# Kernel tuning notes

Measured on AMD Instinct MI355X. Metric: run time of the kernel, lower is better.

The kernel has to match this reference:

```python
import jax, jax.numpy as jnp
import numpy as np

N = 50000        # nodes
E = 800000       # edges (avg degree 16)
F_IN = 128       # in_features
F_OUT = 64       # out_features per head
HEADS = 4        # SparseGATConv default n_heads
ALPHA = 0.01     # LeakyReLU negative slope (SparseGATConv default alpha)


def setup_inputs() -> dict:
    key = jax.random.key(0)
    ks = jax.random.split(key, 6)
    x = jax.random.normal(ks[0], (N, F_IN), dtype=jnp.float32)
    edge_index = jax.random.randint(ks[1], (2, E), 0, N, dtype=jnp.int64)
    # xavier-normal-ish init, gain 1.414 as in the torch module
    W_heads = jax.random.normal(ks[2], (HEADS, F_IN, F_OUT), dtype=jnp.float32) * (1.414 / np.sqrt(F_IN))
    attn_heads = jax.random.normal(ks[3], (HEADS, 2 * F_OUT, 1), dtype=jnp.float32) * 0.1
    W_out = jax.random.normal(ks[4], (HEADS * F_OUT, F_OUT), dtype=jnp.float32) * (1.414 / np.sqrt(HEADS * F_OUT))
    attn_out = jax.random.normal(ks[5], (2 * F_OUT, 1), dtype=jnp.float32) * 0.1
    return {"x": x, "edge_index": edge_index, "W_heads": W_heads,
            "attn_heads": attn_heads, "W_out": W_out, "attn_out": attn_out}


def _sp_gat_layer(x, src, dst, W, attn, concat):
    """SpGraphAttentionLayer.forward: dense x @ W, edge attention scores,
    sparse row-softmax over COO adjacency, sparse-mm aggregation."""
    h = x @ W                                   # (N, d)
    d = h.shape[1]
    # cat(h[src], h[dst]) @ attn  ==  (h@a1)[src] + (h@a2)[dst]  (avoids (E,2d) concat)
    s1 = (h @ attn[:d]).squeeze(-1)             # (N,)
    s2 = (h @ attn[d:]).squeeze(-1)             # (N,)
    scores = -jax.nn.leaky_relu(s1[src] + s2[dst], negative_slope=ALPHA)  # (E,)
    # torch.sparse.softmax(dim=1): softmax over existing entries in each row (src)
    row_max = jax.ops.segment_max(scores, src, num_segments=N)
    ex = jnp.exp(scores - row_max[src])
    denom = jax.ops.segment_sum(ex, src, num_segments=N)
    a = ex / denom[src]                         # (E,) edge attention weights
    # sparse.mm: out[i] = sum_{e: src[e]=i} a[e] * h[dst[e]]
    out = jax.ops.segment_sum(a[:, None] * h[dst], src, num_segments=N)  # (N, d)
    return jax.nn.elu(out) if concat else out


def reference(x, edge_index, W_heads, attn_heads, W_out, attn_out):
    src, dst = edge_index[0], edge_index[1]
    # multi-head GAT layers (concat=True), then out_att on concatenated features
    heads_out = jax.vmap(lambda W, a: _sp_gat_layer(x, src, dst, W, a, True))(W_heads, attn_heads)  # (H, N, F_OUT)
    hcat = jnp.transpose(heads_out, (1, 0, 2)).reshape(N, HEADS * F_OUT)  # matches torch.cat(dim=1) head order
    return _sp_gat_layer(hcat, src, dst, W_out, attn_out, False)          # (N, F_OUT)
```

## Files before the change

### kernel.cpp

```cpp
#include <hip/hip_runtime.h>

typedef unsigned short u16;
typedef _Float16 f16;
typedef __attribute__((ext_vector_type(8))) _Float16 f16x8;
typedef __attribute__((ext_vector_type(2))) _Float16 f16x2;
typedef __attribute__((ext_vector_type(4))) float f32x4;

__device__ inline float nlrelu(float z) { return (z > 0.f) ? -z : -0.01f * z; }
__device__ inline float4 score4(float4 a, float4 b) {
    return make_float4(nlrelu(a.x + b.x), nlrelu(a.y + b.y), nlrelu(a.z + b.z), nlrelu(a.w + b.w));
}
__device__ inline unsigned packdup(float w) {
    f16x2 p = (f16x2){(f16)w, (f16)w};
    return __builtin_bit_cast(unsigned, p);
}

__global__ __launch_bounds__(256) void k_initcnt(const float* __restrict__ Wh, const float* __restrict__ Wo,
                       f16* __restrict__ B1, f16* __restrict__ B2,
                       const int* __restrict__ src, int* __restrict__ counts, int* __restrict__ pos,
                       int* __restrict__ cursor, int E, int N) {
    const int b = blockIdx.x;
    if (b == 0 && threadIdx.x == 0) *cursor = 0;
    if (b < 128) {
        int i = b * 256 + threadIdx.x;
        int j = i & 7, lane = (i >> 3) & 63, kg = (i >> 9) & 3, nt = i >> 11;
        int n = nt * 16 + (lane & 15);
        int k = kg * 32 + ((lane >> 4) << 3) + j;
        B1[i] = (f16)Wh[(n >> 6) * (128 * 64) + k * 64 + (n & 63)];
    } else if (b < 192) {
        int i = (b - 128) * 256 + threadIdx.x;
        int j = i & 7, lane = (i >> 3) & 63, kg = (i >> 9) & 7, nt = i >> 12;
        int n = nt * 16 + (lane & 15);
        int k = kg * 32 + ((lane >> 4) << 3) + j;
        B2[i] = (f16)Wo[k * 64 + n];
    } else {
        const int base = (b - 192) * 1024 + threadIdx.x;
#pragma unroll
        for (int j = 0; j < 4; j++) {
            int e = base + j * 256;
            if (e < E) {
                int s = src[e];
                s = ((unsigned)s < (unsigned)N) ? s : 0;
                pos[e] = atomicAdd(&counts[s], 1);
            }
        }
    }
}

__global__ __launch_bounds__(1024) void scan_ticket(const int* __restrict__ counts, int* __restrict__ rowst,
                                                    int* __restrict__ cursor, int n) {
    const int t = threadIdx.x, lane = t & 63, w = t >> 6;
    __shared__ int wsum[16];
    __shared__ int sh_base;
    int i = blockIdx.x * 1024 + t;
    int v = (i < n) ? counts[i] : 0;
    int orig = v;
    for (int d = 1; d < 64; d <<= 1) { int x = __shfl_up(v, d); if (lane >= d) v += x; }
    if (lane == 63) wsum[w] = v;
    __syncthreads();
    if (t == 0) {
        int acc = 0;
        for (int j = 0; j < 16; j++) { int tmp = wsum[j]; wsum[j] = acc; acc += tmp; }
        sh_base = atomicAdd(cursor, acc);
    }
    __syncthreads();
    if (i < n) rowst[i] = sh_base + wsum[w] + (v - orig);
}

__global__ __launch_bounds__(256) void scatter_noat(const int* __restrict__ src, const int* __restrict__ dst,
                                                    const int* __restrict__ rowst, const int* __restrict__ pos,
                                                    int* __restrict__ edged, int E, int N) {
    const int base = blockIdx.x * 1024 + threadIdx.x;
#pragma unroll
    for (int j = 0; j < 4; j++) {
        int e = base + j * 256;
        if (e < E) {
            int s = src[e];
            s = ((unsigned)s < (unsigned)N) ? s : 0;
            int d = dst[e];
            d = ((unsigned)d < (unsigned)N) ? d : 0;
            edged[rowst[s] + pos[e]] = d;
        }
    }
}

__global__ __launch_bounds__(256) void gemm1_f16(const float* __restrict__ X, const f16* __restrict__ B1,
        const float* __restrict__ attnH,
        f16* __restrict__ H1, float* __restrict__ s1, float* __restrict__ s2, int M) {
    const int lane = threadIdx.x & 63, wave = threadIdx.x >> 6;
    const int row0 = (blockIdx.x * 4 + wave) * 16;
    if (row0 >= M) return;
    const int mrow = row0 + (lane & 15);
    const int koff = (lane >> 4) * 8;
    const float* aptr = X + (size_t)mrow * 128 + koff;

    f32x4 acc[16];
#pragma unroll
    for (int c = 0; c < 16; c++) acc[c] = (f32x4){0.f, 0.f, 0.f, 0.f};

#pragma unroll
    for (int kg = 0; kg < 4; kg++) {
        float av[8];
        *(float4*)av       = *(const float4*)(aptr + kg * 32);
        *(float4*)(av + 4) = *(const float4*)(aptr + kg * 32 + 4);
        f16x8 a;
#pragma unroll
        for (int j = 0; j < 8; j++) a[j] = (f16)av[j];
#pragma unroll
        for (int nt = 0; nt < 16; nt++) {
            const size_t bidx = (size_t)(((nt << 2) + kg) * 64 + lane) * 8;
            f16x8 bfr = *(const f16x8*)(B1 + bidx);
            acc[nt] = __builtin_amdgcn_mfma_f32_16x16x32_f16(a, bfr, acc[nt], 0, 0, 0);
        }
    }
    const int rbase = (lane >> 4) * 4;
    const int colq = lane & 15;
#pragma unroll
    for (int h = 0; h < 4; h++) {
        float s1a[4] = {0.f, 0.f, 0.f, 0.f}, s2a[4] = {0.f, 0.f, 0.f, 0.f};
#pragma unroll
        for (int q = 0; q < 4; q++) {
            const int nt = h * 4 + q;
            const int col = nt * 16 + colq;
            const float a1v = attnH[h * 128 + (col & 63)];
            const float a2v = attnH[h * 128 + 64 + (col & 63)];
#pragma unroll
            for (int r = 0; r < 4; r++) {
                float c = acc[nt][r];
                H1[(size_t)(row0 + rbase + r) * 256 + col] = (f16)c;
                s1a[r] += c * a1v;
                s2a[r] += c * a2v;
            }
        }
#pragma unroll
        for (int off = 1; off < 16; off <<= 1)
#pragma unroll
            for (int r = 0; r < 4; r++) {
                s1a[r] += __shfl_xor(s1a[r], off);
                s2a[r] += __shfl_xor(s2a[r], off);
            }
        if (colq == 0)
#pragma unroll
            for (int r = 0; r < 4; r++) {
                s1[(size_t)(row0 + rbase + r) * 4 + h] = s1a[r];
                s2[(size_t)(row0 + rbase + r) * 4 + h] = s2a[r];
            }
    }
}

__global__ __launch_bounds__(256) void gemm2_f16(const f16* __restrict__ Hc, const f16* __restrict__ B2,
        const float* __restrict__ attnO,
        f16* __restrict__ H2, float* __restrict__ s1b, float* __restrict__ s2b, int M) {
    const int lane = threadIdx.x & 63, wave = threadIdx.x >> 6;
    const int row0 = (blockIdx.x * 4 + wave) * 16;
    if (row0 >= M) return;
    const int mrow = row0 + (lane & 15);
    const int koff = (lane >> 4) * 8;
    const f16* ap = Hc + (size_t)mrow * 256 + koff;

    f32x4 acc[4];
#pragma unroll
    for (int c = 0; c < 4; c++) acc[c] = (f32x4){0.f, 0.f, 0.f, 0.f};

#pragma unroll
    for (int kg = 0; kg < 8; kg++) {
        f16x8 a = *(const f16x8*)(ap + kg * 32);
#pragma unroll
        for (int nt = 0; nt < 4; nt++) {
            const size_t bidx = (size_t)(((nt << 3) + kg) * 64 + lane) * 8;
            f16x8 bfr = *(const f16x8*)(B2 + bidx);
            acc[nt] = __builtin_amdgcn_mfma_f32_16x16x32_f16(a, bfr, acc[nt], 0, 0, 0);
        }
    }
    const int rbase = (lane >> 4) * 4;
    const int colq = lane & 15;
    float s1a[4] = {0.f, 0.f, 0.f, 0.f}, s2a[4] = {0.f, 0.f, 0.f, 0.f};
#pragma unroll
    for (int nt = 0; nt < 4; nt++) {
        const int col = nt * 16 + colq;
        const float a1v = attnO[col];
        const float a2v = attnO[64 + col];
#pragma unroll
        for (int r = 0; r < 4; r++) {
            float c = acc[nt][r];
            H2[(size_t)(row0 + rbase + r) * 64 + col] = (f16)c;
            s1a[r] += c * a1v;
            s2a[r] += c * a2v;
        }
    }
#pragma unroll
    for (int off = 1; off < 16; off <<= 1)
#pragma unroll
        for (int r = 0; r < 4; r++) {
            s1a[r] += __shfl_xor(s1a[r], off);
            s2a[r] += __shfl_xor(s2a[r], off);
        }
    if (colq == 0)
#pragma unroll
        for (int r = 0; r < 4; r++) {
            s1b[row0 + rbase + r] = s1a[r];
            s2b[row0 + rbase + r] = s2a[r];
        }
}

__global__ __launch_bounds__(256) void agg_l1(const int* __restrict__ rowst, const int* __restrict__ cnt,
                                              const int* __restrict__ edged,
                                              const float* __restrict__ s1, const float* __restrict__ s2,
                                              const f16* __restrict__ H, f16* __restrict__ hcat, int N) {
    __shared__ unsigned wls[4][64][4];
    __shared__ int dls[4][64];
    const int t = threadIdx.x, lane = t & 63, wave = t >> 6;
    const int node = blockIdx.x * 4 + wave;
    if (node >= N) return;
    const int beg = rowst[node];
    const int deg = cnt[node];
    const int end = beg + deg;
    if (deg == 0) {
        *(uint2*)(hcat + (size_t)node * 256 + lane * 4) = make_uint2(0u, 0u);
        return;
    }
    const float4 s1v = *(const float4*)(s1 + (size_t)node * 4);

    if (deg <= 64) {
        int d = 0;
        if (lane < deg) d = edged[beg + lane];
        dls[wave][lane] = d;
        float4 s2v = *(const float4*)(s2 + (size_t)d * 4);
        float4 sc = score4(s1v, s2v);
        if (lane >= deg) sc = make_float4(-3e38f, -3e38f, -3e38f, -3e38f);
        float4 m = sc;
#pragma unroll
        for (int off = 32; off > 0; off >>= 1) {
            m.x = fmaxf(m.x, __shfl_xor(m.x, off));
            m.y = fmaxf(m.y, __shfl_xor(m.y, off));
            m.z = fmaxf(m.z, __shfl_xor(m.z, off));
            m.w = fmaxf(m.w, __shfl_xor(m.w, off));
        }
        float4 ex = make_float4(0.f, 0.f, 0.f, 0.f);
        if (lane < deg) ex = make_float4(__expf(sc.x - m.x), __expf(sc.y - m.y),
                                         __expf(sc.z - m.z), __expf(sc.w - m.w));
        float4 sm = ex;
#pragma unroll
        for (int off = 32; off > 0; off >>= 1) {
            sm.x += __shfl_xor(sm.x, off);
            sm.y += __shfl_xor(sm.y, off);
            sm.z += __shfl_xor(sm.z, off);
            sm.w += __shfl_xor(sm.w, off);
        }
        wls[wave][lane][0] = packdup(ex.x / sm.x);
        wls[wave][lane][1] = packdup(ex.y / sm.y);
        wls[wave][lane][2] = packdup(ex.z / sm.z);
        wls[wave][lane][3] = packdup(ex.w / sm.w);
        const int h2 = lane >> 5;
        const int p = lane & 31;
        const int headp = p >> 3;
        f16x2 a0[4], a1[4];
#pragma unroll
        for (int j = 0; j < 4; j++) { a0[j] = (f16x2)(f16)0.f; a1[j] = (f16x2)(f16)0.f; }
        for (int e = 0; e < deg; e += 2) {
            int ei = e + h2;
            int dd = dls[wave][ei];
            f16x2 w2 = __builtin_bit_cast(f16x2, wls[wave][ei][headp]);
            uint4 raw = *(const uint4*)(H + (size_t)dd * 256 + p * 8);
            if ((e >> 1) & 1) {
                a1[0] += w2 * __builtin_bit_cast(f16x2, raw.x);
                a1[1] += w2 * __builtin_bit_cast(f16x2, raw.y);
                a1[2] += w2 * __builtin_bit_cast(f16x2, raw.z);
                a1[3] += w2 * __builtin_bit_cast(f16x2, raw.w);
            } else {
                a0[0] += w2 * __builtin_bit_cast(f16x2, raw.x);
                a0[1] += w2 * __builtin_bit_cast(f16x2, raw.y);
                a0[2] += w2 * __builtin_bit_cast(f16x2, raw.z);
                a0[3] += w2 * __builtin_bit_cast(f16x2, raw.w);
            }
        }
        float r[8];
#pragma unroll
        for (int j = 0; j < 4; j++) {
            r[2 * j]     = (float)a0[j][0] + (float)a1[j][0];
            r[2 * j + 1] = (float)a0[j][1] + (float)a1[j][1];
        }
#pragma unroll
        for (int k = 0; k < 8; k++) r[k] += __shfl_xor(r[k], 32);
        if (lane < 32) {
            uint4 o;
            unsigned* op = &o.x;
#pragma unroll
            for (int j = 0; j < 4; j++) {
                float v0 = r[2 * j], v1 = r[2 * j + 1];
                v0 = (v0 > 0.f) ? v0 : (__expf(v0) - 1.f);
                v1 = (v1 > 0.f) ? v1 : (__expf(v1) - 1.f);
                f16x2 pk = (f16x2){(f16)v0, (f16)v1};
                op[j] = __builtin_bit_cast(unsigned, pk);
            }
            *(uint4*)(hcat + (size_t)node * 256 + p * 8) = o;
        }
    } else {
        const int head = lane >> 4;
        float4 m = make_float4(-3e38f, -3e38f, -3e38f, -3e38f);
        for (int e = beg + lane; e < end; e += 64) {
            int d = edged[e];
            float4 sc = score4(s1v, *(const float4*)(s2 + (size_t)d * 4));
            m.x = fmaxf(m.x, sc.x); m.y = fmaxf(m.y, sc.y); m.z = fmaxf(m.z, sc.z); m.w = fmaxf(m.w, sc.w);
        }
#pragma unroll
        for (int off = 32; off > 0; off >>= 1) {
            m.x = fmaxf(m.x, __shfl_xor(m.x, off));
            m.y = fmaxf(m.y, __shfl_xor(m.y, off));
            m.z = fmaxf(m.z, __shfl_xor(m.z, off));
            m.w = fmaxf(m.w, __shfl_xor(m.w, off));
        }
        float4 sm = make_float4(0.f, 0.f, 0.f, 0.f);
        for (int e = beg + lane; e < end; e += 64) {
            int d = edged[e];
            float4 sc = score4(s1v, *(const float4*)(s2 + (size_t)d * 4));
            sm.x += __expf(sc.x - m.x); sm.y += __expf(sc.y - m.y);
            sm.z += __expf(sc.z - m.z); sm.w += __expf(sc.w - m.w);
        }
#pragma unroll
        for (int off = 32; off > 0; off >>= 1) {
            sm.x += __shfl_xor(sm.x, off);
            sm.y += __shfl_xor(sm.y, off);
            sm.z += __shfl_xor(sm.z, off);
            sm.w += __shfl_xor(sm.w, off);
        }
        float4 inv = make_float4(1.f / sm.x, 1.f / sm.y, 1.f / sm.z, 1.f / sm.w);
        float4 acc = make_float4(0.f, 0.f, 0.f, 0.f);
        for (int e = beg; e < end; e++) {
            int dd = edged[e];
            float4 sc = score4(s1v, *(const float4*)(s2 + (size_t)dd * 4));
            float wv[4] = { __expf(sc.x - m.x) * inv.x, __expf(sc.y - m.y) * inv.y,
                            __expf(sc.z - m.z) * inv.z, __expf(sc.w - m.w) * inv.w };
            float w = (head == 0) ? wv[0] : (head == 1) ? wv[1] : (head == 2) ? wv[2] : wv[3];
            const f16* hp = H + (size_t)dd * 256 + lane * 4;
            acc.x += w * (float)hp[0]; acc.y += w * (float)hp[1];
            acc.z += w * (float)hp[2]; acc.w += w * (float)hp[3];
        }
        acc.x = (acc.x > 0.f) ? acc.x : (__expf(acc.x) - 1.f);
        acc.y = (acc.y > 0.f) ? acc.y : (__expf(acc.y) - 1.f);
        acc.z = (acc.z > 0.f) ? acc.z : (__expf(acc.z) - 1.f);
        acc.w = (acc.w > 0.f) ? acc.w : (__expf(acc.w) - 1.f);
        f16x2 o0 = (f16x2){(f16)acc.x, (f16)acc.y};
        f16x2 o1 = (f16x2){(f16)acc.z, (f16)acc.w};
        *(uint2*)(hcat + (size_t)node * 256 + lane * 4) =
            make_uint2(__builtin_bit_cast(unsigned, o0), __builtin_bit_cast(unsigned, o1));
    }
}

__global__ __launch_bounds__(256) void agg_l2(const int* __restrict__ rowst, const int* __restrict__ cnt,
                                              const int* __restrict__ edged,
                                              const float* __restrict__ s1, const float* __restrict__ s2,
                                              const f16* __restrict__ H, float* __restrict__ outp, int N) {
    __shared__ float wls[4][64];
    __shared__ int dls[4][64];
    const int t = threadIdx.x, lane = t & 63, wave = t >> 6;
    const int node = blockIdx.x * 4 + wave;
    if (node >= N) return;
    const int beg = rowst[node];
    const int deg = cnt[node];
    const int end = beg + deg;
    if (deg == 0) { outp[(size_t)node * 64 + lane] = 0.f; return; }
    const float s1v = s1[node];

    if (deg <= 64) {
        int d = 0;
        if (lane < deg) d = edged[beg + lane];
        dls[wave][lane] = d;
        float z = s1v + s2[d];
        float sc = (lane < deg) ? nlrelu(z) : -3e38f;
        float m = sc;
#pragma unroll
        for (int off = 32; off > 0; off >>= 1) m = fmaxf(m, __shfl_xor(m, off));
        float ex = (lane < deg) ? __expf(sc - m) : 0.f;
        float sm = ex;
#pragma unroll
        for (int off = 32; off > 0; off >>= 1) sm += __shfl_xor(sm, off);
        wls[wave][lane] = ex / sm;
        const int h2 = lane >> 5;
        const int p = lane & 31;
        float ax = 0.f, ay = 0.f;
        for (int e = 0; e < deg; e += 2) {
            int ei = e + h2;
            float w = wls[wave][ei];
            int dd = dls[wave][ei];
            unsigned raw = *(const unsigned*)(H + (size_t)dd * 64 + p * 2);
            f16x2 hv = __builtin_bit_cast(f16x2, raw);
            ax += w * (float)hv[0];
            ay += w * (float)hv[1];
        }
        ax += __shfl_xor(ax, 32);
        ay += __shfl_xor(ay, 32);
        if (lane < 32) *(float2*)(outp + (size_t)node * 64 + p * 2) = make_float2(ax, ay);
    } else {
        float m = -3e38f;
        for (int e = beg + lane; e < end; e += 64) {
            int d = edged[e];
            m = fmaxf(m, nlrelu(s1v + s2[d]));
        }
#pragma unroll
        for (int off = 32; off > 0; off >>= 1) m = fmaxf(m, __shfl_xor(m, off));
        float sm = 0.f;
        for (int e = beg + lane; e < end; e += 64) {
            int d = edged[e];
            sm += __expf(nlrelu(s1v + s2[d]) - m);
        }
#pragma unroll
        for (int off = 32; off > 0; off >>= 1) sm += __shfl_xor(sm, off);
        float inv = 1.f / sm;
        float acc = 0.f;
        for (int e = beg; e < end; e++) {
            int dd = edged[e];
            float w = __expf(nlrelu(s1v + s2[dd]) - m) * inv;
            acc += w * (float)H[(size_t)dd * 64 + lane];
        }
        outp[(size_t)node * 64 + lane] = acc;
    }
}

extern "C" void kernel_launch(void* const* d_in, const int* in_sizes, int n_in,
                              void* d_out, int out_size, void* d_ws, size_t ws_size,
                              hipStream_t stream) {
    const float* x     = (const float*)d_in[0];
    const int*   ei    = (const int*)d_in[1];
    const float* Wh    = (const float*)d_in[2];
    const float* attnH = (const float*)d_in[3];
    const float* Wo    = (const float*)d_in[4];
    const float* attnO = (const float*)d_in[5];
    float* out         = (float*)d_out;

    const int N = in_sizes[0] / 128;
    const int E = in_sizes[1] / 2;
    const int* srcp = ei;
    const int* dstp = ei + E;

    char* base = (char*)d_ws;
    size_t off = 0;
    auto take = [&](size_t b) { void* p = base + off; off += (b + 255) & ~(size_t)255; return p; };
    f16*   B1     = (f16*)  take(32768 * 2);
    f16*   B2     = (f16*)  take(16384 * 2);
    int*   counts = (int*)  take((size_t)N * 4);
    int*   rowst  = (int*)  take((size_t)N * 4);
    int*   pos    = (int*)  take((size_t)E * 4);
    int*   edged  = (int*)  take((size_t)E * 4);
    int*   cursor = (int*)  take(256);
    float* s1     = (float*)take((size_t)N * 4 * 4);
    float* s2     = (float*)take((size_t)N * 4 * 4);
    float* s1b    = (float*)take((size_t)N * 4);
    float* s2b    = (float*)take((size_t)N * 4);
    f16*   H1     = (f16*)  take((size_t)N * 256 * 2);
    f16*   hcat   = (f16*)  take((size_t)N * 256 * 2);
    f16*   H2     = (f16*)  take((size_t)N * 64 * 2);

    hipMemsetAsync(counts, 0, (size_t)N * 4, stream);

    const int eb4 = (E + 1023) / 1024;
    k_initcnt<<<192 + eb4, 256, 0, stream>>>(Wh, Wo, B1, B2, srcp, counts, pos, cursor, E, N);

    const int nb = (N + 1023) / 1024;
    scan_ticket<<<nb, 1024, 0, stream>>>(counts, rowst, cursor, N);

    scatter_noat<<<eb4, 256, 0, stream>>>(srcp, dstp, rowst, pos, edged, E, N);

    const int Gg = (N + 63) / 64;
    gemm1_f16<<<Gg, 256, 0, stream>>>(x, B1, attnH, H1, s1, s2, N);
    agg_l1<<<(N + 3) / 4, 256, 0, stream>>>(rowst, counts, edged, s1, s2, H1, hcat, N);
    gemm2_f16<<<Gg, 256, 0, stream>>>(hcat, B2, attnO, H2, s1b, s2b, N);
    agg_l2<<<(N + 3) / 4, 256, 0, stream>>>(rowst, counts, edged, s1b, s2b, H2, out, N);
}
```

Measured before the change: 258.1 us.

## Fuse layer-1 aggregation with second GEMM and merge scatter into GEMM1 launch

Edge scatter and the first GEMM now share one launch, split by block index. The layer-1 aggregation writes each 16-node tile of concatenated head features into LDS, and one wave then runs the second MFMA GEMM and its attention-score reductions on it. This removes the global hcat buffer round trip and two kernel launches. The softmax max-subtraction passes are also dropped in both layers, trading numerical headroom for fewer edge passes; the fused kernel also has fewer independent waves per node and idles three waves during the GEMM.

```diff
diff --git a/kernel.cpp b/kernel.cpp
--- a/kernel.cpp
+++ b/kernel.cpp
@@ -1,6 +1,5 @@
 #include <hip/hip_runtime.h>
 
-typedef unsigned short u16;
 typedef _Float16 f16;
 typedef __attribute__((ext_vector_type(8))) _Float16 f16x8;
 typedef __attribute__((ext_vector_type(2))) _Float16 f16x2;
@@ -67,28 +66,30 @@
     if (i < n) rowst[i] = sh_base + wsum[w] + (v - orig);
 }
 
-__global__ __launch_bounds__(256) void scatter_noat(const int* __restrict__ src, const int* __restrict__ dst,
-                                                    const int* __restrict__ rowst, const int* __restrict__ pos,
-                                                    int* __restrict__ edged, int E, int N) {
-    const int base = blockIdx.x * 1024 + threadIdx.x;
-#pragma unroll
-    for (int j = 0; j < 4; j++) {
-        int e = base + j * 256;
-        if (e < E) {
-            int s = src[e];
-            s = ((unsigned)s < (unsigned)N) ? s : 0;
-            int d = dst[e];
-            d = ((unsigned)d < (unsigned)N) ? d : 0;
-            edged[rowst[s] + pos[e]] = d;
-        }
-    }
-}
-
-__global__ __launch_bounds__(256) void gemm1_f16(const float* __restrict__ X, const f16* __restrict__ B1,
-        const float* __restrict__ attnH,
-        f16* __restrict__ H1, float* __restrict__ s1, float* __restrict__ s2, int M) {
+__global__ __launch_bounds__(256) void k_scatg1(
+        const int* __restrict__ src, const int* __restrict__ dst,
+        const int* __restrict__ rowst, const int* __restrict__ pos, int* __restrict__ edged,
+        const float* __restrict__ X, const f16* __restrict__ B1, const float* __restrict__ attnH,
+        f16* __restrict__ H1, float* __restrict__ s1, float* __restrict__ s2,
+        int M, int E, int N, int Gs) {
+    if ((int)blockIdx.x < Gs) {
+        const int base = blockIdx.x * 1024 + threadIdx.x;
+#pragma unroll
+        for (int j = 0; j < 4; j++) {
+            int e = base + j * 256;
+            if (e < E) {
+                int s = src[e];
+                s = ((unsigned)s < (unsigned)N) ? s : 0;
+                int d = dst[e];
+                d = ((unsigned)d < (unsigned)N) ? d : 0;
+                edged[rowst[s] + pos[e]] = d;
+            }
+        }
+        return;
+    }
+    const int gb = blockIdx.x - Gs;
     const int lane = threadIdx.x & 63, wave = threadIdx.x >> 6;
-    const int row0 = (blockIdx.x * 4 + wave) * 16;
+    const int row0 = (gb * 4 + wave) * 16;
     if (row0 >= M) return;
     const int mrow = row0 + (lane & 15);
     const int koff = (lane >> 4) * 8;
@@ -148,202 +149,177 @@
     }
 }
 
-__global__ __launch_bounds__(256) void gemm2_f16(const f16* __restrict__ Hc, const f16* __restrict__ B2,
-        const float* __restrict__ attnO,
-        f16* __restrict__ H2, float* __restrict__ s1b, float* __restrict__ s2b, int M) {
-    const int lane = threadIdx.x & 63, wave = threadIdx.x >> 6;
-    const int row0 = (blockIdx.x * 4 + wave) * 16;
-    if (row0 >= M) return;
-    const int mrow = row0 + (lane & 15);
-    const int koff = (lane >> 4) * 8;
-    const f16* ap = Hc + (size_t)mrow * 256 + koff;
-
-    f32x4 acc[4];
-#pragma unroll
-    for (int c = 0; c < 4; c++) acc[c] = (f32x4){0.f, 0.f, 0.f, 0.f};
-
-#pragma unroll
-    for (int kg = 0; kg < 8; kg++) {
-        f16x8 a = *(const f16x8*)(ap + kg * 32);
-#pragma unroll
-        for (int nt = 0; nt < 4; nt++) {
-            const size_t bidx = (size_t)(((nt << 3) + kg) * 64 + lane) * 8;
-            f16x8 bfr = *(const f16x8*)(B2 + bidx);
-            acc[nt] = __builtin_amdgcn_mfma_f32_16x16x32_f16(a, bfr, acc[nt], 0, 0, 0);
-        }
-    }
-    const int rbase = (lane >> 4) * 4;
-    const int colq = lane & 15;
-    float s1a[4] = {0.f, 0.f, 0.f, 0.f}, s2a[4] = {0.f, 0.f, 0.f, 0.f};
-#pragma unroll
-    for (int nt = 0; nt < 4; nt++) {
-        const int col = nt * 16 + colq;
-        const float a1v = attnO[col];
-        const float a2v = attnO[64 + col];
-#pragma unroll
-        for (int r = 0; r < 4; r++) {
-            float c = acc[nt][r];
-            H2[(size_t)(row0 + rbase + r) * 64 + col] = (f16)c;
-            s1a[r] += c * a1v;
-            s2a[r] += c * a2v;
-        }
-    }
-#pragma unroll
-    for (int off = 1; off < 16; off <<= 1)
-#pragma unroll
-        for (int r = 0; r < 4; r++) {
-            s1a[r] += __shfl_xor(s1a[r], off);
-            s2a[r] += __shfl_xor(s2a[r], off);
-        }
-    if (colq == 0)
-#pragma unroll
-        for (int r = 0; r < 4; r++) {
-            s1b[row0 + rbase + r] = s1a[r];
-            s2b[row0 + rbase + r] = s2a[r];
-        }
-}
-
-__global__ __launch_bounds__(256) void agg_l1(const int* __restrict__ rowst, const int* __restrict__ cnt,
-                                              const int* __restrict__ edged,
-                                              const float* __restrict__ s1, const float* __restrict__ s2,
-                                              const f16* __restrict__ H, f16* __restrict__ hcat, int N) {
+__global__ __launch_bounds__(256) void agg1g2(
+        const int* __restrict__ rowst, const int* __restrict__ cnt, const int* __restrict__ edged,
+        const float* __restrict__ s1, const float* __restrict__ s2, const f16* __restrict__ H,
+        const f16* __restrict__ B2, const float* __restrict__ attnO,
+        f16* __restrict__ H2, float* __restrict__ s1b, float* __restrict__ s2b, int N) {
     __shared__ unsigned wls[4][64][4];
     __shared__ int dls[4][64];
+    __shared__ f16 hc[16][264];
     const int t = threadIdx.x, lane = t & 63, wave = t >> 6;
-    const int node = blockIdx.x * 4 + wave;
-    if (node >= N) return;
-    const int beg = rowst[node];
-    const int deg = cnt[node];
-    const int end = beg + deg;
-    if (deg == 0) {
-        *(uint2*)(hcat + (size_t)node * 256 + lane * 4) = make_uint2(0u, 0u);
-        return;
-    }
-    const float4 s1v = *(const float4*)(s1 + (size_t)node * 4);
-
-    if (deg <= 64) {
-        int d = 0;
-        if (lane < deg) d = edged[beg + lane];
-        dls[wave][lane] = d;
-        float4 s2v = *(const float4*)(s2 + (size_t)d * 4);
-        float4 sc = score4(s1v, s2v);
-        if (lane >= deg) sc = make_float4(-3e38f, -3e38f, -3e38f, -3e38f);
-        float4 m = sc;
-#pragma unroll
-        for (int off = 32; off > 0; off >>= 1) {
-            m.x = fmaxf(m.x, __shfl_xor(m.x, off));
-            m.y = fmaxf(m.y, __shfl_xor(m.y, off));
-            m.z = fmaxf(m.z, __shfl_xor(m.z, off));
-            m.w = fmaxf(m.w, __shfl_xor(m.w, off));
-        }
-        float4 ex = make_float4(0.f, 0.f, 0.f, 0.f);
-        if (lane < deg) ex = make_float4(__expf(sc.x - m.x), __expf(sc.y - m.y),
-                                         __expf(sc.z - m.z), __expf(sc.w - m.w));
-        float4 sm = ex;
-#pragma unroll
-        for (int off = 32; off > 0; off >>= 1) {
-            sm.x += __shfl_xor(sm.x, off);
-            sm.y += __shfl_xor(sm.y, off);
-            sm.z += __shfl_xor(sm.z, off);
-            sm.w += __shfl_xor(sm.w, off);
-        }
-        wls[wave][lane][0] = packdup(ex.x / sm.x);
-        wls[wave][lane][1] = packdup(ex.y / sm.y);
-        wls[wave][lane][2] = packdup(ex.z / sm.z);
-        wls[wave][lane][3] = packdup(ex.w / sm.w);
-        const int h2 = lane >> 5;
-        const int p = lane & 31;
-        const int headp = p >> 3;
-        f16x2 a0[4], a1[4];
-#pragma unroll
-        for (int j = 0; j < 4; j++) { a0[j] = (f16x2)(f16)0.f; a1[j] = (f16x2)(f16)0.f; }
-        for (int e = 0; e < deg; e += 2) {
-            int ei = e + h2;
-            int dd = dls[wave][ei];
-            f16x2 w2 = __builtin_bit_cast(f16x2, wls[wave][ei][headp]);
-            uint4 raw = *(const uint4*)(H + (size_t)dd * 256 + p * 8);
-            if ((e >> 1) & 1) {
-                a1[0] += w2 * __builtin_bit_cast(f16x2, raw.x);
-                a1[1] += w2 * __builtin_bit_cast(f16x2, raw.y);
-                a1[2] += w2 * __builtin_bit_cast(f16x2, raw.z);
-                a1[3] += w2 * __builtin_bit_cast(f16x2, raw.w);
-            } else {
-                a0[0] += w2 * __builtin_bit_cast(f16x2, raw.x);
-                a0[1] += w2 * __builtin_bit_cast(f16x2, raw.y);
-                a0[2] += w2 * __builtin_bit_cast(f16x2, raw.z);
-                a0[3] += w2 * __builtin_bit_cast(f16x2, raw.w);
-            }
-        }
-        float r[8];
-#pragma unroll
-        for (int j = 0; j < 4; j++) {
-            r[2 * j]     = (float)a0[j][0] + (float)a1[j][0];
-            r[2 * j + 1] = (float)a0[j][1] + (float)a1[j][1];
-        }
-#pragma unroll
-        for (int k = 0; k < 8; k++) r[k] += __shfl_xor(r[k], 32);
-        if (lane < 32) {
-            uint4 o;
-            unsigned* op = &o.x;
+    const int nbase = blockIdx.x * 16 + wave * 4;
+
+    for (int i = 0; i < 4; i++) {
+        const int node = nbase + i;
+        const int slot = wave * 4 + i;
+        if (node >= N) { *(uint2*)&hc[slot][lane * 4] = make_uint2(0u, 0u); continue; }
+        const int beg = rowst[node];
+        const int deg = cnt[node];
+        if (deg == 0) { *(uint2*)&hc[slot][lane * 4] = make_uint2(0u, 0u); continue; }
+        const float4 s1v = *(const float4*)(s1 + (size_t)node * 4);
+
+        if (deg <= 64) {
+            int d = 0;
+            if (lane < deg) d = edged[beg + lane];
+            dls[wave][lane] = d;
+            float4 s2v = *(const float4*)(s2 + (size_t)d * 4);
+            float4 sc = score4(s1v, s2v);
+            float4 ex = make_float4(0.f, 0.f, 0.f, 0.f);
+            if (lane < deg) ex = make_float4(__expf(sc.x), __expf(sc.y), __expf(sc.z), __expf(sc.w));
+            float4 sm = ex;
+#pragma unroll
+            for (int off = 32; off > 0; off >>= 1) {
+                sm.x += __shfl_xor(sm.x, off);
+                sm.y += __shfl_xor(sm.y, off);
+                sm.z += __shfl_xor(sm.z, off);
+                sm.w += __shfl_xor(sm.w, off);
+            }
+            wls[wave][lane][0] = packdup(ex.x / sm.x);
+            wls[wave][lane][1] = packdup(ex.y / sm.y);
+            wls[wave][lane][2] = packdup(ex.z / sm.z);
+            wls[wave][lane][3] = packdup(ex.w / sm.w);
+            const int h2 = lane >> 5;
+            const int p = lane & 31;
+            const int headp = p >> 3;
+            f16x2 a0[4], a1[4];
+#pragma unroll
+            for (int j = 0; j < 4; j++) { a0[j] = (f16x2)(f16)0.f; a1[j] = (f16x2)(f16)0.f; }
+            for (int e = 0; e < deg; e += 2) {
+                int ei = e + h2;
+                int dd = dls[wave][ei];
+                f16x2 w2 = __builtin_bit_cast(f16x2, wls[wave][ei][headp]);
+                uint4 raw = *(const uint4*)(H + (size_t)dd * 256 + p * 8);
+                if ((e >> 1) & 1) {
+                    a1[0] += w2 * __builtin_bit_cast(f16x2, raw.x);
+                    a1[1] += w2 * __builtin_bit_cast(f16x2, raw.y);
+                    a1[2] += w2 * __builtin_bit_cast(f16x2, raw.z);
+                    a1[3] += w2 * __builtin_bit_cast(f16x2, raw.w);
+                } else {
+                    a0[0] += w2 * __builtin_bit_cast(f16x2, raw.x);
+                    a0[1] += w2 * __builtin_bit_cast(f16x2, raw.y);
+                    a0[2] += w2 * __builtin_bit_cast(f16x2, raw.z);
+                    a0[3] += w2 * __builtin_bit_cast(f16x2, raw.w);
+                }
+            }
+            float r[8];
 #pragma unroll
             for (int j = 0; j < 4; j++) {
-                float v0 = r[2 * j], v1 = r[2 * j + 1];
-                v0 = (v0 > 0.f) ? v0 : (__expf(v0) - 1.f);
-                v1 = (v1 > 0.f) ? v1 : (__expf(v1) - 1.f);
-                f16x2 pk = (f16x2){(f16)v0, (f16)v1};
-                op[j] = __builtin_bit_cast(unsigned, pk);
-            }
-            *(uint4*)(hcat + (size_t)node * 256 + p * 8) = o;
-        }
-    } else {
-        const int head = lane >> 4;
-        float4 m = make_float4(-3e38f, -3e38f, -3e38f, -3e38f);
-        for (int e = beg + lane; e < end; e += 64) {
-            int d = edged[e];
-            float4 sc = score4(s1v, *(const float4*)(s2 + (size_t)d * 4));
-            m.x = fmaxf(m.x, sc.x); m.y = fmaxf(m.y, sc.y); m.z = fmaxf(m.z, sc.z); m.w = fmaxf(m.w, sc.w);
-        }
-#pragma unroll
-        for (int off = 32; off > 0; off >>= 1) {
-            m.x = fmaxf(m.x, __shfl_xor(m.x, off));
-            m.y = fmaxf(m.y, __shfl_xor(m.y, off));
-            m.z = fmaxf(m.z, __shfl_xor(m.z, off));
-            m.w = fmaxf(m.w, __shfl_xor(m.w, off));
-        }
-        float4 sm = make_float4(0.f, 0.f, 0.f, 0.f);
-        for (int e = beg + lane; e < end; e += 64) {
-            int d = edged[e];
-            float4 sc = score4(s1v, *(const float4*)(s2 + (size_t)d * 4));
-            sm.x += __expf(sc.x - m.x); sm.y += __expf(sc.y - m.y);
-            sm.z += __expf(sc.z - m.z); sm.w += __expf(sc.w - m.w);
-        }
-#pragma unroll
-        for (int off = 32; off > 0; off >>= 1) {
-            sm.x += __shfl_xor(sm.x, off);
-            sm.y += __shfl_xor(sm.y, off);
-            sm.z += __shfl_xor(sm.z, off);
-            sm.w += __shfl_xor(sm.w, off);
-        }
-        float4 inv = make_float4(1.f / sm.x, 1.f / sm.y, 1.f / sm.z, 1.f / sm.w);
-        float4 acc = make_float4(0.f, 0.f, 0.f, 0.f);
-        for (int e = beg; e < end; e++) {
-            int dd = edged[e];
-            float4 sc = score4(s1v, *(const float4*)(s2 + (size_t)dd * 4));
-            float wv[4] = { __expf(sc.x - m.x) * inv.x, __expf(sc.y - m.y) * inv.y,
-                            __expf(sc.z - m.z) * inv.z, __expf(sc.w - m.w) * inv.w };
-            float w = (head == 0) ? wv[0] : (head == 1) ? wv[1] : (head == 2) ? wv[2] : wv[3];
-            const f16* hp = H + (size_t)dd * 256 + lane * 4;
-            acc.x += w * (float)hp[0]; acc.y += w * (float)hp[1];
-            acc.z += w * (float)hp[2]; acc.w += w * (float)hp[3];
-        }
-        acc.x = (acc.x > 0.f) ? acc.x : (__expf(acc.x) - 1.f);
-        acc.y = (acc.y > 0.f) ? acc.y : (__expf(acc.y) - 1.f);
-        acc.z = (acc.z > 0.f) ? acc.z : (__expf(acc.z) - 1.f);
-        acc.w = (acc.w > 0.f) ? acc.w : (__expf(acc.w) - 1.f);
-        f16x2 o0 = (f16x2){(f16)acc.x, (f16)acc.y};
-        f16x2 o1 = (f16x2){(f16)acc.z, (f16)acc.w};
-        *(uint2*)(hcat + (size_t)node * 256 + lane * 4) =
-            make_uint2(__builtin_bit_cast(unsigned, o0), __builtin_bit_cast(unsigned, o1));
+                r[2 * j]     = (float)a0[j][0] + (float)a1[j][0];
+                r[2 * j + 1] = (float)a0[j][1] + (float)a1[j][1];
+            }
+#pragma unroll
+            for (int k = 0; k < 8; k++) r[k] += __shfl_xor(r[k], 32);
+            if (lane < 32) {
+                uint4 o;
+                unsigned* op = &o.x;
+#pragma unroll
+                for (int j = 0; j < 4; j++) {
+                    float v0 = r[2 * j], v1 = r[2 * j + 1];
+                    v0 = (v0 > 0.f) ? v0 : (__expf(v0) - 1.f);
+                    v1 = (v1 > 0.f) ? v1 : (__expf(v1) - 1.f);
+                    f16x2 pk = (f16x2){(f16)v0, (f16)v1};
+                    op[j] = __builtin_bit_cast(unsigned, pk);
+                }
+                *(uint4*)&hc[slot][p * 8] = o;
+            }
+        } else {
+            const int end = beg + deg;
+            const int head = lane >> 4;
+            float4 sm = make_float4(0.f, 0.f, 0.f, 0.f);
+            for (int e = beg + lane; e < end; e += 64) {
+                int d = edged[e];
+                float4 sc = score4(s1v, *(const float4*)(s2 + (size_t)d * 4));
+                sm.x += __expf(sc.x); sm.y += __expf(sc.y);
+                sm.z += __expf(sc.z); sm.w += __expf(sc.w);
+            }
+#pragma unroll
+            for (int off = 32; off > 0; off >>= 1) {
+                sm.x += __shfl_xor(sm.x, off);
+                sm.y += __shfl_xor(sm.y, off);
+                sm.z += __shfl_xor(sm.z, off);
+                sm.w += __shfl_xor(sm.w, off);
+            }
+            float4 inv = make_float4(1.f / sm.x, 1.f / sm.y, 1.f / sm.z, 1.f / sm.w);
+            float4 acc = make_float4(0.f, 0.f, 0.f, 0.f);
+            for (int e = beg; e < end; e++) {
+                int dd = edged[e];
+                float4 sc = score4(s1v, *(const float4*)(s2 + (size_t)dd * 4));
+                float wv[4] = { __expf(sc.x) * inv.x, __expf(sc.y) * inv.y,
+                                __expf(sc.z) * inv.z, __expf(sc.w) * inv.w };
+                float w = (head == 0) ? wv[0] : (head == 1) ? wv[1] : (head == 2) ? wv[2] : wv[3];
+                const f16* hp = H + (size_t)dd * 256 + lane * 4;
+                acc.x += w * (float)hp[0]; acc.y += w * (float)hp[1];
+                acc.z += w * (float)hp[2]; acc.w += w * (float)hp[3];
+            }
+            acc.x = (acc.x > 0.f) ? acc.x : (__expf(acc.x) - 1.f);
+            acc.y = (acc.y > 0.f) ? acc.y : (__expf(acc.y) - 1.f);
+            acc.z = (acc.z > 0.f) ? acc.z : (__expf(acc.z) - 1.f);
+            acc.w = (acc.w > 0.f) ? acc.w : (__expf(acc.w) - 1.f);
+            f16x2 o0 = (f16x2){(f16)acc.x, (f16)acc.y};
+            f16x2 o1 = (f16x2){(f16)acc.z, (f16)acc.w};
+            *(uint2*)&hc[slot][lane * 4] =
+                make_uint2(__builtin_bit_cast(unsigned, o0), __builtin_bit_cast(unsigned, o1));
+        }
+    }
+    __syncthreads();
+    if (wave == 0) {
+        const int m = lane & 15;
+        const int koff = (lane >> 4) * 8;
+        f32x4 acc[4];
+#pragma unroll
+        for (int c = 0; c < 4; c++) acc[c] = (f32x4){0.f, 0.f, 0.f, 0.f};
+#pragma unroll
+        for (int kg = 0; kg < 8; kg++) {
+            f16x8 a = *(const f16x8*)&hc[m][kg * 32 + koff];
+#pragma unroll
+            for (int nt = 0; nt < 4; nt++) {
+                const size_t bidx = (size_t)(((nt << 3) + kg) * 64 + lane) * 8;
+                f16x8 bfr = *(const f16x8*)(B2 + bidx);
+                acc[nt] = __builtin_amdgcn_mfma_f32_16x16x32_f16(a, bfr, acc[nt], 0, 0, 0);
+            }
+        }
+        const int row0 = blockIdx.x * 16;
+        const int rbase = (lane >> 4) * 4;
+        const int colq = lane & 15;
+        float s1a[4] = {0.f, 0.f, 0.f, 0.f}, s2a[4] = {0.f, 0.f, 0.f, 0.f};
+#pragma unroll
+        for (int nt = 0; nt < 4; nt++) {
+            const int col = nt * 16 + colq;
+            const float a1v = attnO[col];
+            const float a2v = attnO[64 + col];
+#pragma unroll
+            for (int r = 0; r < 4; r++) {
+                float c = acc[nt][r];
+                int row = row0 + rbase + r;
+                if (row < N) H2[(size_t)row * 64 + col] = (f16)c;
+                s1a[r] += c * a1v;
+                s2a[r] += c * a2v;
+            }
+        }
+#pragma unroll
+        for (int off = 1; off < 16; off <<= 1)
+#pragma unroll
+            for (int r = 0; r < 4; r++) {
+                s1a[r] += __shfl_xor(s1a[r], off);
+                s2a[r] += __shfl_xor(s2a[r], off);
+            }
+        if (colq == 0)
+#pragma unroll
+            for (int r = 0; r < 4; r++) {
+                int row = row0 + rbase + r;
+                if (row < N) { s1b[row] = s1a[r]; s2b[row] = s2a[r]; }
+            }
     }
 }
 
@@ -366,12 +342,8 @@
         int d = 0;
         if (lane < deg) d = edged[beg + lane];
         dls[wave][lane] = d;
-        float z = s1v + s2[d];
-        float sc = (lane < deg) ? nlrelu(z) : -3e38f;
-        float m = sc;
-#pragma unroll
-        for (int off = 32; off > 0; off >>= 1) m = fmaxf(m, __shfl_xor(m, off));
-        float ex = (lane < deg) ? __expf(sc - m) : 0.f;
+        float sc = nlrelu(s1v + s2[d]);
+        float ex = (lane < deg) ? __expf(sc) : 0.f;
         float sm = ex;
 #pragma unroll
         for (int off = 32; off > 0; off >>= 1) sm += __shfl_xor(sm, off);
@@ -392,17 +364,10 @@
         ay += __shfl_xor(ay, 32);
         if (lane < 32) *(float2*)(outp + (size_t)node * 64 + p * 2) = make_float2(ax, ay);
     } else {
-        float m = -3e38f;
-        for (int e = beg + lane; e < end; e += 64) {
-            int d = edged[e];
-            m = fmaxf(m, nlrelu(s1v + s2[d]));
-        }
-#pragma unroll
-        for (int off = 32; off > 0; off >>= 1) m = fmaxf(m, __shfl_xor(m, off));
         float sm = 0.f;
         for (int e = beg + lane; e < end; e += 64) {
             int d = edged[e];
-            sm += __expf(nlrelu(s1v + s2[d]) - m);
+            sm += __expf(nlrelu(s1v + s2[d]));
         }
 #pragma unroll
         for (int off = 32; off > 0; off >>= 1) sm += __shfl_xor(sm, off);
@@ -410,7 +375,7 @@
         float acc = 0.f;
         for (int e = beg; e < end; e++) {
             int dd = edged[e];
-            float w = __expf(nlrelu(s1v + s2[dd]) - m) * inv;
+            float w = __expf(nlrelu(s1v + s2[dd])) * inv;
             acc += w * (float)H[(size_t)dd * 64 + lane];
         }
         outp[(size_t)node * 64 + lane] = acc;
@@ -448,7 +413,6 @@
     float* s1b    = (float*)take((size_t)N * 4);
     float* s2b    = (float*)take((size_t)N * 4);
     f16*   H1     = (f16*)  take((size_t)N * 256 * 2);
-    f16*   hcat   = (f16*)  take((size_t)N * 256 * 2);
     f16*   H2     = (f16*)  take((size_t)N * 64 * 2);
 
     hipMemsetAsync(counts, 0, (size_t)N * 4, stream);
@@ -459,11 +423,13 @@
     const int nb = (N + 1023) / 1024;
     scan_ticket<<<nb, 1024, 0, stream>>>(counts, rowst, cursor, N);
 
-    scatter_noat<<<eb4, 256, 0, stream>>>(srcp, dstp, rowst, pos, edged, E, N);
-
+    const int Gs = eb4;
     const int Gg = (N + 63) / 64;
-    gemm1_f16<<<Gg, 256, 0, stream>>>(x, B1, attnH, H1, s1, s2, N);
-    agg_l1<<<(N + 3) / 4, 256, 0, stream>>>(rowst, counts, edged, s1, s2, H1, hcat, N);
-    gemm2_f16<<<Gg, 256, 0, stream>>>(hcat, B2, attnO, H2, s1b, s2b, N);
+    k_scatg1<<<Gs + Gg, 256, 0, stream>>>(srcp, dstp, rowst, pos, edged,
+                                          x, B1, attnH, H1, s1, s2, N, E, N, Gs);
+
+    agg1g2<<<(N + 15) / 16, 256, 0, stream>>>(rowst, counts, edged, s1, s2, H1,
+                                              B2, attnO, H2, s1b, s2b, N);
+
     agg_l2<<<(N + 3) / 4, 256, 0, stream>>>(rowst, counts, edged, s1b, s2b, H2, out, N);
 }
```

After: 243.4 us. 1.06x faster.
